# Performance work log

Hardware: AMD Instinct MI355X
Metric: run time of the kernel (lower is better)

## Reference

```python
import jax, jax.numpy as jnp
from jax import lax
import numpy as np


def tridiagonal_solve(K, f):
    """Batched Thomas-algorithm solve of A(K) u = f.

    K: [..., m] diffusion coefficient at m grid points.
    f: broadcastable to [..., m-1] right-hand side.
    Returns u: [..., m-1].
    """
    n = K.shape[-1] - 1  # number of unknowns
    h2 = 1.0 / (n * n)
    f = jnp.broadcast_to(f, (*K.shape[:-1], n))

    denom0 = 2.0 * K[..., 0] + K[..., 1]
    c0 = -K[..., 1] / denom0  # [...]
    u0 = f[..., 0] / denom0

    # Forward elimination sweep, j = 1 .. n-2, as a scan over the grid axis.
    Kj = jnp.moveaxis(K[..., 1:n - 1], -1, 0)   # [n-2, ...] = K[..., j]
    Kj1 = jnp.moveaxis(K[..., 2:n], -1, 0)      # [n-2, ...] = K[..., j+1]
    fj = jnp.moveaxis(f[..., 1:n - 1], -1, 0)   # [n-2, ...]

    def fwd_step(carry, x):
        c_prev, u_prev = carry
        kj, kj1, fv = x
        denom = kj + kj1 + kj * c_prev
        c = -kj1 / denom
        u = (fv + kj * u_prev) / denom
        return (c, u), (c, u)

    _, (cs, us) = lax.scan(fwd_step, (c0, u0), (Kj, Kj1, fj))
    c_all = jnp.concatenate([c0[None], cs], axis=0)  # [n-1, ...] indices 0..n-2
    u_all = jnp.concatenate([u0[None], us], axis=0)  # [n-1, ...]

    Kn1 = K[..., n - 1]
    u_last = (f[..., n - 1] + Kn1 * u_all[-1]) / (Kn1 + Kn1 * c_all[-1])  # u[n-1]

    # Back substitution: u[j] -= c[j] * u[j+1], j = n-2 .. 0 (reverse scan).
    def bwd_step(u_next, x):
        cj, uj = x
        u_new = uj - cj * u_next
        return u_new, u_new

    _, u_head = lax.scan(bwd_step, u_last, (c_all, u_all), reverse=True)  # [n-1, ...]
    u_full = jnp.concatenate([u_head, u_last[None]], axis=0)  # [n, ...]
    return h2 * jnp.moveaxis(u_full, 0, -1)


def setup_inputs() -> dict:
    key = jax.random.key(0)
    k1, k2 = jax.random.split(key)
    B, M = 16384, 1024  # batch, grid points (n = M - 1 unknowns)
    alpha = jax.random.normal(k1, (B, M), dtype=jnp.float32)
    f_rhs = jax.random.normal(k2, (M - 1,), dtype=jnp.float32)
    return {"alpha": alpha, "f_rhs": f_rhs}


def reference(alpha, f_rhs):
    # DiffusionModel1d.forward: u = A(exp(alpha))^{-1} f_rhs
    return tridiagonal_solve(jnp.exp(alpha), f_rhs)
```

## Files before the change

kernel.cpp:

```cpp
#include <hip/hip_runtime.h>
#include <math.h>


constexpr int BT   = 16384;
constexpr int MPTS = 1024;
constexpr int NU   = 1023;
constexpr int CS   = 16;
constexpr int P    = 64;
constexpr int WPB  = 4;

__device__ __forceinline__ double fast_rcp(double x) {
    double r = (double)__builtin_amdgcn_rcpf((float)x);
    r = r * fma(-x, r, 2.0);
    r = r * fma(-x, r, 2.0);
    return r;
}

__global__ __launch_bounds__(WPB * 64)
void pt_kernel(const float* __restrict__ alpha,
               const float* __restrict__ f_rhs,
               float* __restrict__ out) {
    const int t    = threadIdx.x;
    const int lane = t & 63;
    const int w    = t >> 6;
    const int row  = blockIdx.x * WPB + w;
    const int s    = lane * CS;

    __shared__ float ostage[WPB][NU + (NU >> 5) + 2];

    const float* arow = alpha + (size_t)row * MPTS;
    float kf[CS + 1];
    #pragma unroll
    for (int q = 0; q < 4; ++q) {
        const float4 v = *reinterpret_cast<const float4*>(arow + s + 4 * q);
        kf[4 * q + 0] = expf(v.x);
        kf[4 * q + 1] = expf(v.y);
        kf[4 * q + 2] = expf(v.z);
        kf[4 * q + 3] = expf(v.w);
    }
    {
        float kx = (lane < P - 1) ? arow[s + CS] : 0.0f;
        kf[CS] = expf(kx);
    }

    float ff[CS];
    #pragma unroll
    for (int q = 0; q < 3; ++q) {
        const float4 v = *reinterpret_cast<const float4*>(f_rhs + s + 4 * q);
        ff[4 * q + 0] = v.x; ff[4 * q + 1] = v.y;
        ff[4 * q + 2] = v.z; ff[4 * q + 3] = v.w;
    }
    if (lane < P - 1) {
        const float4 v = *reinterpret_cast<const float4*>(f_rhs + s + 12);
        ff[12] = v.x; ff[13] = v.y; ff[14] = v.z; ff[15] = v.w;
    } else {
        ff[12] = f_rhs[1020]; ff[13] = f_rhs[1021]; ff[14] = f_rhs[1022];
        ff[15] = 0.0f;
    }

    double cA[CS], uA[CS], vA[CS];
    {
        double cp = 0.0, up = 0.0, vp = 1.0;
        #pragma unroll
        for (int i = 0; i < CS; ++i) {
            const int j = s + i;
            const double kc = (double)kf[i];
            const double kn = (double)kf[i + 1];
            double a, b, d;
            double f = (double)ff[i];
            if (j == 0)            { a = 0.0;  b = 2.0 * kc + kn; d = -kn; }
            else if (j == NU - 1)  { a = -kc;  b = kc;            d = 0.0; }
            else if (j == NU)      { a = 0.0;  b = 1.0;           d = 0.0; f = 0.0; }
            else                   { a = -kc;  b = kc + kn;       d = -kn; }
            const double den = fma(-a, cp, b);
            const double r   = fast_rcp(den);
            const double ci  = d * r;
            const double ui  = fma(-a, up, f) * r;
            const double vi  = (-a * vp) * r;
            cA[i] = ci; uA[i] = ui; vA[i] = vi;
            cp = ci; up = ui; vp = vi;
        }
    }

    double De, Ae, Be;
    {
        double Dn = uA[CS - 1], An = vA[CS - 1], Bn = -cA[CS - 1];
        De = Dn; Ae = An; Be = Bn;
        uA[CS - 1] = Dn; vA[CS - 1] = An; cA[CS - 1] = Bn;
        #pragma unroll
        for (int i = CS - 2; i >= 0; --i) {
            const double ci = cA[i];
            Dn = fma(-ci, Dn, uA[i]);
            An = fma(-ci, An, vA[i]);
            Bn = -ci * Bn;
            uA[i] = Dn; vA[i] = An; cA[i] = Bn;
        }
    }
    const double Ds = uA[0], As = vA[0], Bs = cA[0];

    double m00 = Bs;
    double m01 = fma(Bs, De, -(Ds * Be));
    double m02 = Ds;
    double m11 = fma(Bs, Ae, -(As * Be));
    double m12 = As;
    double m21 = -Be;
    double m22 = 1.0;

    #pragma unroll
    for (int dlt = 1; dlt < 64; dlt <<= 1) {
        const bool val = (lane + dlt) < 64;
        double b00 = __shfl_down(m00, dlt); b00 = val ? b00 : 1.0;
        double b01 = __shfl_down(m01, dlt); b01 = val ? b01 : 0.0;
        double b02 = __shfl_down(m02, dlt); b02 = val ? b02 : 0.0;
        double b11 = __shfl_down(m11, dlt); b11 = val ? b11 : 1.0;
        double b12 = __shfl_down(m12, dlt); b12 = val ? b12 : 0.0;
        double b21 = __shfl_down(m21, dlt); b21 = val ? b21 : 0.0;
        double b22 = __shfl_down(m22, dlt); b22 = val ? b22 : 1.0;
        const double n00 = m00 * b00;
        const double n01 = fma(m00, b01, fma(m01, b11, m02 * b21));
        const double n02 = fma(m00, b02, fma(m01, b12, m02 * b22));
        const double n11 = fma(m11, b11, m12 * b21);
        const double n12 = fma(m11, b12, m12 * b22);
        const double n21 = fma(m21, b11, m22 * b21);
        const double n22 = fma(m21, b12, m22 * b22);
        const double rn = fast_rcp(n22);
        m00 = n00 * rn; m01 = n01 * rn; m02 = n02 * rn;
        m11 = n11 * rn; m12 = n12 * rn;
        m21 = n21 * rn; m22 = n22 * rn;
    }
    const double rmm = fast_rcp(m22);
    const double alf = m02 * rmm;
    const double bet = m12 * rmm;
    double alfn = __shfl_down(alf, 1); alfn = (lane == 63) ? 0.0 : alfn;
    double betn = __shfl_down(bet, 1); betn = (lane == 63) ? 0.0 : betn;

    const double tt = fast_rcp(fma(-Be, betn, 1.0));
    const double dl = fma(Be, alfn, De) * tt;
    const double gm = Ae * tt;

    double X = dl, G = gm;
    #pragma unroll
    for (int dlt = 1; dlt < 64; dlt <<= 1) {
        double bx = __shfl_up(X, dlt);
        double bg = __shfl_up(G, dlt);
        const bool val = lane >= dlt;
        bx = val ? bx : 0.0;
        bg = val ? bg : 1.0;
        X = fma(G, bx, X);
        G = G * bg;
    }
    double xp = __shfl_up(X, 1);
    const double uL = (lane == 0) ? 0.0 : xp;
    const double Y  = fma(bet, uL, alf);
    double yn = __shfl_down(Y, 1);
    const double uR = (lane == 63) ? 0.0 : yn;

    const double h2 = 1.0 / (1023.0 * 1023.0);
    float* ost = ostage[w];
    #pragma unroll
    for (int i = 0; i < CS; ++i) {
        const int j = s + i;
        const double uu = fma(vA[i], uL, fma(cA[i], uR, uA[i]));
        if (j < NU) ost[j + (j >> 5)] = (float)(h2 * uu);
    }
    __syncthreads();

    float* orow = out + (size_t)row * NU;
    #pragma unroll
    for (int it = 0; it < 16; ++it) {
        const int c = it * 64 + lane;
        if (c < NU) orow[c] = ost[c + (c >> 5)];
    }
}

extern "C" void kernel_launch(void* const* d_in, const int* in_sizes, int n_in,
                              void* d_out, int out_size, void* d_ws, size_t ws_size,
                              hipStream_t stream) {
    const float* alpha = (const float*)d_in[0];
    const float* f_rhs = (const float*)d_in[1];
    float* out = (float*)d_out;

    dim3 grid(BT / WPB), block(WPB * 64);
    pt_kernel<<<grid, block, 0, stream>>>(alpha, f_rhs, out);
}
```

Measured before the change: 45.37 us.

## Simplify tridiagonal sweep boundaries, stage f in LDS, drop normalized matrix entry

```diff
diff --git a/kernel.cpp b/kernel.cpp
--- a/kernel.cpp
+++ b/kernel.cpp
@@ -6,17 +6,15 @@
 constexpr int MPTS = 1024;
 constexpr int NU   = 1023;
 constexpr int CS   = 16;
-constexpr int P    = 64;
 constexpr int WPB  = 4;
 
 __device__ __forceinline__ double fast_rcp(double x) {
-    double r = (double)__builtin_amdgcn_rcpf((float)x);
-    r = r * fma(-x, r, 2.0);
-    r = r * fma(-x, r, 2.0);
+    double r = __builtin_amdgcn_rcp(x);
+    r = fma(r, fma(-x, r, 1.0), r);
     return r;
 }
 
-__global__ __launch_bounds__(WPB * 64)
+__global__ __launch_bounds__(WPB * 64, 3)
 void pt_kernel(const float* __restrict__ alpha,
                const float* __restrict__ f_rhs,
                float* __restrict__ out) {
@@ -27,6 +25,10 @@
     const int s    = lane * CS;
 
     __shared__ float ostage[WPB][NU + (NU >> 5) + 2];
+    __shared__ float f_lds[1056];
+
+    for (int i = t; i < NU; i += WPB * 64) f_lds[i + (i >> 5)] = f_rhs[i];
+    if (t == 0) f_lds[1023 + (1023 >> 5)] = 0.0f;
 
     const float* arow = alpha + (size_t)row * MPTS;
     float kf[CS + 1];
@@ -39,50 +41,36 @@
         kf[4 * q + 3] = expf(v.w);
     }
     {
-        float kx = (lane < P - 1) ? arow[s + CS] : 0.0f;
+        float kx = (lane < 63) ? arow[s + CS] : 0.0f;
         kf[CS] = expf(kx);
     }
+    if (lane == 63) kf[15] = 0.0f;
 
-    float ff[CS];
-    #pragma unroll
-    for (int q = 0; q < 3; ++q) {
-        const float4 v = *reinterpret_cast<const float4*>(f_rhs + s + 4 * q);
-        ff[4 * q + 0] = v.x; ff[4 * q + 1] = v.y;
-        ff[4 * q + 2] = v.z; ff[4 * q + 3] = v.w;
-    }
-    if (lane < P - 1) {
-        const float4 v = *reinterpret_cast<const float4*>(f_rhs + s + 12);
-        ff[12] = v.x; ff[13] = v.y; ff[14] = v.z; ff[15] = v.w;
-    } else {
-        ff[12] = f_rhs[1020]; ff[13] = f_rhs[1021]; ff[14] = f_rhs[1022];
-        ff[15] = 0.0f;
-    }
+    __syncthreads();
 
     double cA[CS], uA[CS], vA[CS];
     {
-        double cp = 0.0, up = 0.0, vp = 1.0;
+        double cp = (lane == 0) ? 1.0 : 0.0;
+        double up = 0.0, vp = 1.0;
         #pragma unroll
         for (int i = 0; i < CS; ++i) {
             const int j = s + i;
             const double kc = (double)kf[i];
             const double kn = (double)kf[i + 1];
-            double a, b, d;
-            double f = (double)ff[i];
-            if (j == 0)            { a = 0.0;  b = 2.0 * kc + kn; d = -kn; }
-            else if (j == NU - 1)  { a = -kc;  b = kc;            d = 0.0; }
-            else if (j == NU)      { a = 0.0;  b = 1.0;           d = 0.0; f = 0.0; }
-            else                   { a = -kc;  b = kc + kn;       d = -kn; }
-            const double den = fma(-a, cp, b);
+            const double b  = kc + kn;
+            const double f  = (double)f_lds[j + (j >> 5)];
+            const double den = fma(kc, cp, b);
             const double r   = fast_rcp(den);
-            const double ci  = d * r;
-            const double ui  = fma(-a, up, f) * r;
-            const double vi  = (-a * vp) * r;
+            double ci = -kn * r;
+            const double ui = fma(kc, up, f) * r;
+            const double vi = (kc * vp) * r;
+            if (i == CS - 1) ci = (lane == 63) ? 0.0 : ci;
             cA[i] = ci; uA[i] = ui; vA[i] = vi;
             cp = ci; up = ui; vp = vi;
         }
     }
 
-    double De, Ae, Be;
+    double De, Ae, Be, Ds, As, Bs;
     {
         double Dn = uA[CS - 1], An = vA[CS - 1], Bn = -cA[CS - 1];
         De = Dn; Ae = An; Be = Bn;
@@ -95,8 +83,8 @@
             Bn = -ci * Bn;
             uA[i] = Dn; vA[i] = An; cA[i] = Bn;
         }
+        Ds = uA[0]; As = vA[0]; Bs = cA[0];
     }
-    const double Ds = uA[0], As = vA[0], Bs = cA[0];
 
     double m00 = Bs;
     double m01 = fma(Bs, De, -(Ds * Be));
@@ -104,7 +92,6 @@
     double m11 = fma(Bs, Ae, -(As * Be));
     double m12 = As;
     double m21 = -Be;
-    double m22 = 1.0;
 
     #pragma unroll
     for (int dlt = 1; dlt < 64; dlt <<= 1) {
@@ -115,22 +102,19 @@
         double b11 = __shfl_down(m11, dlt); b11 = val ? b11 : 1.0;
         double b12 = __shfl_down(m12, dlt); b12 = val ? b12 : 0.0;
         double b21 = __shfl_down(m21, dlt); b21 = val ? b21 : 0.0;
-        double b22 = __shfl_down(m22, dlt); b22 = val ? b22 : 1.0;
         const double n00 = m00 * b00;
         const double n01 = fma(m00, b01, fma(m01, b11, m02 * b21));
-        const double n02 = fma(m00, b02, fma(m01, b12, m02 * b22));
+        const double n02 = fma(m00, b02, fma(m01, b12, m02));
         const double n11 = fma(m11, b11, m12 * b21);
-        const double n12 = fma(m11, b12, m12 * b22);
-        const double n21 = fma(m21, b11, m22 * b21);
-        const double n22 = fma(m21, b12, m22 * b22);
+        const double n12 = fma(m11, b12, m12);
+        const double n21 = fma(m21, b11, b21);
+        const double n22 = fma(m21, b12, 1.0);
         const double rn = fast_rcp(n22);
         m00 = n00 * rn; m01 = n01 * rn; m02 = n02 * rn;
-        m11 = n11 * rn; m12 = n12 * rn;
-        m21 = n21 * rn; m22 = n22 * rn;
+        m11 = n11 * rn; m12 = n12 * rn; m21 = n21 * rn;
     }
-    const double rmm = fast_rcp(m22);
-    const double alf = m02 * rmm;
-    const double bet = m12 * rmm;
+    const double alf = m02;
+    const double bet = m12;
     double alfn = __shfl_down(alf, 1); alfn = (lane == 63) ? 0.0 : alfn;
     double betn = __shfl_down(bet, 1); betn = (lane == 63) ? 0.0 : betn;
 
```

Result: faster. 42.97 us (-5.3%).
